# Kernel tuning notes

Measured on AMD Instinct MI355X. Metric: run time of the kernel, lower is better.

## Reference

```python
import jax, jax.numpy as jnp
import numpy as np

N_NODES = 50000
N_EDGES = 800000
D_FEAT = 128
HEADS = 4
C_HID = 64   # n_gat_channels
C_LAST = 64  # fixed in module
ALPHA_LRELU = 0.2


def gat_conv(x, tgt, src, W, a_self, a_neigh, b):
    """Spektral GATConv (single/sparse mode, inference, concat_heads=True)."""
    N = x.shape[0]
    xp = jnp.einsum('nf,fhc->nhc', x, W)                 # [N,H,C] per-head projection
    e_self = jnp.einsum('nhc,hc->nh', xp, a_self)        # [N,H]
    e_neigh = jnp.einsum('nhc,hc->nh', xp, a_neigh)      # [N,H]
    e = jax.nn.leaky_relu(e_self[tgt] + e_neigh[src], ALPHA_LRELU)  # [E,H]
    # segment softmax over incoming edges of each target node
    m = jax.ops.segment_max(e, tgt, num_segments=N)
    m = jnp.where(jnp.isfinite(m), m, 0.0)               # guard empty segments
    ex = jnp.exp(e - m[tgt])
    denom = jax.ops.segment_sum(ex, tgt, num_segments=N)
    alpha = ex / denom[tgt]                               # [E,H]
    msg = alpha[:, :, None] * xp[src]                     # [E,H,C]
    out = jax.ops.segment_sum(msg, tgt, num_segments=N)   # [N,H,C]
    out = out.reshape(N, -1) + b                          # concat heads -> [N,H*C]
    return jax.nn.selu(out)


def setup_inputs() -> dict:
    key = jax.random.key(0)
    ks = jax.random.split(key, 16)
    lecun = lambda k, shape, fan_in: jax.random.normal(k, shape, jnp.float32) * np.sqrt(1.0 / fan_in)
    x = jax.random.normal(ks[0], (N_NODES, D_FEAT), jnp.float32)
    edge_index = jax.random.randint(ks[1], (2, N_EDGES), 0, N_NODES, jnp.int64)
    F1 = HEADS * C_HID
    F2 = HEADS * C_LAST
    return {
        'x': x,
        'edge_index': edge_index,
        'W1': lecun(ks[2], (D_FEAT, HEADS, C_HID), D_FEAT),
        'a_self1': lecun(ks[3], (HEADS, C_HID), C_HID),
        'a_neigh1': lecun(ks[4], (HEADS, C_HID), C_HID),
        'b1': jnp.zeros((F1,), jnp.float32),
        'W2': lecun(ks[5], (F1, HEADS, C_LAST), F1),
        'a_self2': lecun(ks[6], (HEADS, C_LAST), C_LAST),
        'a_neigh2': lecun(ks[7], (HEADS, C_LAST), C_LAST),
        'b2': jnp.zeros((F2,), jnp.float32),
        'Wd1': lecun(ks[8], (F2, 64), F2),
        'bd1': jnp.zeros((64,), jnp.float32),
        'Wd2': lecun(ks[9], (64, 32), 64),
        'bd2': jnp.zeros((32,), jnp.float32),
        'Wo': lecun(ks[10], (32, 1), 32),
        'bo': jnp.zeros((1,), jnp.float32),
    }


def reference(x, edge_index, W1, a_self1, a_neigh1, b1, W2, a_self2, a_neigh2, b2,
              Wd1, bd1, Wd2, bd2, Wo, bo):
    tgt, src = edge_index[0], edge_index[1]
    h = gat_conv(x, tgt, src, W1, a_self1, a_neigh1, b1)   # hidden GATConv (dropout=identity)
    h = gat_conv(h, tgt, src, W2, a_self2, a_neigh2, b2)   # last GATConv
    g = h.sum(axis=0)                                      # GlobalSumPool -> [F2]
    g = jax.nn.selu(g @ Wd1 + bd1)
    g = jax.nn.selu(g @ Wd2 + bd2)
    return g @ Wo + bo                                     # [1]
```

## Files before the change

### kernel.cpp

```cpp
#include <hip/hip_runtime.h>
#include <hip/hip_bf16.h>
#include <hip/hip_fp8.h>
#include <math.h>

#define N_NODES 50000
#define N_EDGES 800000
#define SLOT_CAP 96
#define AGG_BLOCKS (N_NODES / 4)

typedef __attribute__((ext_vector_type(8))) short short8;
typedef __attribute__((ext_vector_type(4))) float f32x4;
typedef __attribute__((ext_vector_type(2))) float f32x2;

__device__ __forceinline__ float selu_f(float x) {
    const float scale = 1.0507009873554805f;
    const float alpha = 1.6732632423543772f;
    return x > 0.f ? scale * x : scale * alpha * (expf(x) - 1.f);
}
__device__ __forceinline__ float lrelu_f(float x) {
    return x >= 0.f ? x : 0.2f * x;
}
__device__ __forceinline__ ushort f2bf(float f) {
    __hip_bfloat16 h = __float2bfloat16(f);
    return *(ushort*)&h;
}
__device__ __forceinline__ unsigned char f2fp8(float f) {
    __hip_fp8_e4m3 q(f);
    return (unsigned char)q.__x;
}
__device__ __forceinline__ float fp82f(unsigned char b) {
    __hip_fp8_e4m3 q; q.__x = (__hip_fp8_storage_t)b;
    return (float)q;
}
__device__ __forceinline__ void fp8x4_decode(unsigned u, float* o) {
#if __has_builtin(__builtin_amdgcn_cvt_pk_f32_fp8)
    f32x2 lo = __builtin_amdgcn_cvt_pk_f32_fp8((int)u, false);
    f32x2 hi = __builtin_amdgcn_cvt_pk_f32_fp8((int)u, true);
    o[0] = lo.x; o[1] = lo.y; o[2] = hi.x; o[3] = hi.y;
#else
    o[0] = fp82f(u & 0xff);
    o[1] = fp82f((u >> 8) & 0xff);
    o[2] = fp82f((u >> 16) & 0xff);
    o[3] = fp82f(u >> 24);
#endif
}
__device__ __forceinline__ unsigned fp8x4_encode(float f0, float f1, float f2, float f3) {
#if __has_builtin(__builtin_amdgcn_cvt_pk_fp8_f32)
    int v = 0;
    v = __builtin_amdgcn_cvt_pk_fp8_f32(f0, f1, v, false);
    v = __builtin_amdgcn_cvt_pk_fp8_f32(f2, f3, v, true);
    return (unsigned)v;
#else
    return (unsigned)f2fp8(f0) | ((unsigned)f2fp8(f1) << 8) |
           ((unsigned)f2fp8(f2) << 16) | ((unsigned)f2fp8(f3) << 24);
#endif
}

__global__ void pack_all(const float* __restrict__ x, ushort* __restrict__ Apx,
                         const float* __restrict__ W1, ushort* __restrict__ Bp1,
                         const float* __restrict__ W2, ushort* __restrict__ Bp2,
                         int* __restrict__ cursor, float* __restrict__ g) {
    int i = blockIdx.x * blockDim.x + threadIdx.x;
    if (i < N_NODES * 128 / 8) {
        const float4* p = (const float4*)x + (size_t)i * 2;
        float4 a = p[0], b = p[1];
        ushort u[8] = { f2bf(a.x), f2bf(a.y), f2bf(a.z), f2bf(a.w),
                        f2bf(b.x), f2bf(b.y), f2bf(b.z), f2bf(b.w) };
        *(uint4*)(Apx + (size_t)i * 8) = *(uint4*)u;
    }
    if (i < 16 * 256) {
        int kg = i >> 8, n = i & 255;
        ushort u[8];
#pragma unroll
        for (int j = 0; j < 8; j++) u[j] = f2bf(W1[(size_t)(kg * 8 + j) * 256 + n]);
        *(uint4*)(Bp1 + ((size_t)kg * 256 + n) * 8) = *(uint4*)u;
    }
    if (i < 32 * 256) {
        int kg = i >> 8, n = i & 255;
        ushort u[8];
#pragma unroll
        for (int j = 0; j < 8; j++) u[j] = f2bf(W2[(size_t)(kg * 8 + j) * 256 + n]);
        *(uint4*)(Bp2 + ((size_t)kg * 256 + n) * 8) = *(uint4*)u;
    }
    if (i < N_NODES) cursor[i] = 0;
    if (i < 256) g[i] = 0.f;
}

__global__ void edge_scatter(const int* __restrict__ tgt, const int* __restrict__ src,
                             int* __restrict__ cursor, int* __restrict__ ssrc, int E) {
    int e = blockIdx.x * blockDim.x + threadIdx.x;
    if (e >= E) return;
    int t = tgt[e];
    int r = atomicAdd(&cursor[t], 1);
    if (r < SLOT_CAP) ssrc[(size_t)t * SLOT_CAP + r] = src[e];
}

__global__ __launch_bounds__(256) void gemm_scores(const short8* __restrict__ A,
                                                   const short8* __restrict__ B,
                                                   unsigned char* __restrict__ C,
                                                   const float* __restrict__ a_self,
                                                   const float* __restrict__ a_neigh,
                                                   float* __restrict__ es,
                                                   float* __restrict__ en,
                                                   int K8, int M) {
    __shared__ short8 Atile[64][5];
    const int tid = threadIdx.x;
    const int wv = tid >> 6, lane = tid & 63;
    const int q = lane >> 4, t = lane & 15;
    const int m0 = blockIdx.x * 64;
    const int n0 = wv * 64;

    const int srow = tid >> 2, sc = tid & 3;
    int grow = m0 + srow; if (grow > M - 1) grow = M - 1;
    const short8* Ag = A + (size_t)grow * K8 + sc;

    f32x4 acc[4][4];
#pragma unroll
    for (int mr = 0; mr < 4; mr++)
#pragma unroll
        for (int nc = 0; nc < 4; nc++) acc[mr][nc] = (f32x4){0.f, 0.f, 0.f, 0.f};

    const short8* Bb = B + (size_t)q * 256 + n0 + t;
    for (int kk = 0; kk < K8; kk += 4) {
        __syncthreads();
        Atile[srow][sc] = Ag[kk];
        __syncthreads();
        short8 a0 = Atile[t][q];
        short8 a1 = Atile[16 + t][q];
        short8 a2 = Atile[32 + t][q];
        short8 a3 = Atile[48 + t][q];
        short8 b0 = Bb[(size_t)kk * 256 + 0];
        short8 b1 = Bb[(size_t)kk * 256 + 16];
        short8 b2 = Bb[(size_t)kk * 256 + 32];
        short8 b3 = Bb[(size_t)kk * 256 + 48];
        acc[0][0] = __builtin_amdgcn_mfma_f32_16x16x32_bf16(a0, b0, acc[0][0], 0, 0, 0);
        acc[0][1] = __builtin_amdgcn_mfma_f32_16x16x32_bf16(a0, b1, acc[0][1], 0, 0, 0);
        acc[0][2] = __builtin_amdgcn_mfma_f32_16x16x32_bf16(a0, b2, acc[0][2], 0, 0, 0);
        acc[0][3] = __builtin_amdgcn_mfma_f32_16x16x32_bf16(a0, b3, acc[0][3], 0, 0, 0);
        acc[1][0] = __builtin_amdgcn_mfma_f32_16x16x32_bf16(a1, b0, acc[1][0], 0, 0, 0);
        acc[1][1] = __builtin_amdgcn_mfma_f32_16x16x32_bf16(a1, b1, acc[1][1], 0, 0, 0);
        acc[1][2] = __builtin_amdgcn_mfma_f32_16x16x32_bf16(a1, b2, acc[1][2], 0, 0, 0);
        acc[1][3] = __builtin_amdgcn_mfma_f32_16x16x32_bf16(a1, b3, acc[1][3], 0, 0, 0);
        acc[2][0] = __builtin_amdgcn_mfma_f32_16x16x32_bf16(a2, b0, acc[2][0], 0, 0, 0);
        acc[2][1] = __builtin_amdgcn_mfma_f32_16x16x32_bf16(a2, b1, acc[2][1], 0, 0, 0);
        acc[2][2] = __builtin_amdgcn_mfma_f32_16x16x32_bf16(a2, b2, acc[2][2], 0, 0, 0);
        acc[2][3] = __builtin_amdgcn_mfma_f32_16x16x32_bf16(a2, b3, acc[2][3], 0, 0, 0);
        acc[3][0] = __builtin_amdgcn_mfma_f32_16x16x32_bf16(a3, b0, acc[3][0], 0, 0, 0);
        acc[3][1] = __builtin_amdgcn_mfma_f32_16x16x32_bf16(a3, b1, acc[3][1], 0, 0, 0);
        acc[3][2] = __builtin_amdgcn_mfma_f32_16x16x32_bf16(a3, b2, acc[3][2], 0, 0, 0);
        acc[3][3] = __builtin_amdgcn_mfma_f32_16x16x32_bf16(a3, b3, acc[3][3], 0, 0, 0);
    }

    unsigned char* Cr = C + n0 + t;
#pragma unroll
    for (int mr = 0; mr < 4; mr++) {
#pragma unroll
        for (int r = 0; r < 4; r++) {
            int row = m0 + mr * 16 + q * 4 + r;
            if (row < M) {
                size_t ro = (size_t)row * 256;
                unsigned pk = fp8x4_encode(acc[mr][0][r], acc[mr][1][r],
                                           acc[mr][2][r], acc[mr][3][r]);
                Cr[ro +  0] = (unsigned char)(pk & 0xff);
                Cr[ro + 16] = (unsigned char)((pk >> 8) & 0xff);
                Cr[ro + 32] = (unsigned char)((pk >> 16) & 0xff);
                Cr[ro + 48] = (unsigned char)(pk >> 24);
            }
        }
    }

    float as[4], an[4];
#pragma unroll
    for (int nc = 0; nc < 4; nc++) {
        as[nc] = a_self[n0 + nc * 16 + t];
        an[nc] = a_neigh[n0 + nc * 16 + t];
    }
#pragma unroll
    for (int mr = 0; mr < 4; mr++) {
#pragma unroll
        for (int r = 0; r < 4; r++) {
            float pes = acc[mr][0][r] * as[0] + acc[mr][1][r] * as[1]
                      + acc[mr][2][r] * as[2] + acc[mr][3][r] * as[3];
            float pen = acc[mr][0][r] * an[0] + acc[mr][1][r] * an[1]
                      + acc[mr][2][r] * an[2] + acc[mr][3][r] * an[3];
#pragma unroll
            for (int mask = 1; mask < 16; mask <<= 1) {
                pes += __shfl_xor(pes, mask);
                pen += __shfl_xor(pen, mask);
            }
            if (t == 0) {
                int row = m0 + mr * 16 + q * 4 + r;
                if (row < M) {
                    es[(size_t)row * 4 + wv] = pes;
                    en[(size_t)row * 4 + wv] = pen;
                }
            }
        }
    }
}

__global__ __launch_bounds__(256) void aggregate(const unsigned char* __restrict__ xp,
                                                 const float* __restrict__ es,
                                                 const float* __restrict__ en,
                                                 const int* __restrict__ cursor,
                                                 const int* __restrict__ ssrc,
                                                 const float* __restrict__ bias,
                                                 ushort* __restrict__ out,
                                                 float* __restrict__ partials, int N) {
    __shared__ float part[4][256];
    int wave = (blockIdx.x * blockDim.x + threadIdx.x) >> 6;
    int wv = (threadIdx.x >> 6) & 3;
    int lane = threadIdx.x & 63;
    if (wave >= N) return;
    int n = wave;
    int e0 = n * SLOT_CAP;
    int deg = cursor[n]; deg = (deg > SLOT_CAP) ? SLOT_CAP : deg;
    int e1 = e0 + deg;
    int h = lane >> 4;
    int c0 = lane * 4;
    float esh = es[(size_t)n * 4 + h];
    float dd = 0.f;
    float a0 = 0.f, a1 = 0.f, a2 = 0.f, a3 = 0.f;
    float b0 = 0.f, b1 = 0.f, b2 = 0.f, b3 = 0.f;
    int e = e0;
    for (; e + 1 < e1; e += 2) {
        int sA = __builtin_amdgcn_readfirstlane(ssrc[e]);
        int sB = __builtin_amdgcn_readfirstlane(ssrc[e + 1]);
        float evA = __expf(lrelu_f(esh + en[(size_t)sA * 4 + h]));
        float evB = __expf(lrelu_f(esh + en[(size_t)sB * 4 + h]));
        unsigned uA = *(const unsigned*)(xp + (size_t)sA * 256 + c0);
        unsigned uB = *(const unsigned*)(xp + (size_t)sB * 256 + c0);
        dd += evA + evB;
        float fA[4], fB[4];
        fp8x4_decode(uA, fA);
        fp8x4_decode(uB, fB);
        a0 += evA * fA[0]; a1 += evA * fA[1]; a2 += evA * fA[2]; a3 += evA * fA[3];
        b0 += evB * fB[0]; b1 += evB * fB[1]; b2 += evB * fB[2]; b3 += evB * fB[3];
    }
    if (e < e1) {
        int s = __builtin_amdgcn_readfirstlane(ssrc[e]);
        float ev = __expf(lrelu_f(esh + en[(size_t)s * 4 + h]));
        unsigned u = *(const unsigned*)(xp + (size_t)s * 256 + c0);
        dd += ev;
        float f[4];
        fp8x4_decode(u, f);
        a0 += ev * f[0]; a1 += ev * f[1]; a2 += ev * f[2]; a3 += ev * f[3];
    }
    float inv = (dd > 0.f) ? 1.f / dd : 0.f;
    float4 bb = *(const float4*)(bias + c0);
    float r0 = selu_f((a0 + b0) * inv + bb.x);
    float r1 = selu_f((a1 + b1) * inv + bb.y);
    float r2 = selu_f((a2 + b2) * inv + bb.z);
    float r3 = selu_f((a3 + b3) * inv + bb.w);
    if (partials == nullptr) {
        ushort r[4] = { f2bf(r0), f2bf(r1), f2bf(r2), f2bf(r3) };
        *(uint2*)(out + (size_t)n * 256 + c0) = *(uint2*)r;
    } else {
        part[wv][c0 + 0] = r0; part[wv][c0 + 1] = r1;
        part[wv][c0 + 2] = r2; part[wv][c0 + 3] = r3;
        __syncthreads();
        if (wv == 0) {
            float4 s;
            s.x = r0 + part[1][c0 + 0] + part[2][c0 + 0] + part[3][c0 + 0];
            s.y = r1 + part[1][c0 + 1] + part[2][c0 + 1] + part[3][c0 + 1];
            s.z = r2 + part[1][c0 + 2] + part[2][c0 + 2] + part[3][c0 + 2];
            s.w = r3 + part[1][c0 + 3] + part[2][c0 + 3] + part[3][c0 + 3];
            *(float4*)(partials + (size_t)blockIdx.x * 256 + c0) = s;
        }
    }
}

__global__ __launch_bounds__(256) void colsum_part(const float* __restrict__ p,
                                                   float* __restrict__ g, int R) {
    __shared__ float part[4][256];
    int tid = threadIdx.x;
    int rg = tid >> 6;
    int c0 = (tid & 63) * 4;
    float4 acc = {0.f, 0.f, 0.f, 0.f};
    for (int r = blockIdx.x * 4 + rg; r < R; r += gridDim.x * 4) {
        float4 v = *(const float4*)(p + (size_t)r * 256 + c0);
        acc.x += v.x; acc.y += v.y; acc.z += v.z; acc.w += v.w;
    }
    *(float4*)(&part[rg][c0]) = acc;
    __syncthreads();
    if (rg == 0) {
        float4 s = acc;
        for (int r = 1; r < 4; r++) {
            s.x += part[r][c0 + 0]; s.y += part[r][c0 + 1];
            s.z += part[r][c0 + 2]; s.w += part[r][c0 + 3];
        }
        atomicAdd(&g[c0 + 0], s.x);
        atomicAdd(&g[c0 + 1], s.y);
        atomicAdd(&g[c0 + 2], s.z);
        atomicAdd(&g[c0 + 3], s.w);
    }
}

__global__ __launch_bounds__(256) void mlp_head(const float* __restrict__ g,
                                                const float* __restrict__ Wd1, const float* __restrict__ bd1,
                                                const float* __restrict__ Wd2, const float* __restrict__ bd2,
                                                const float* __restrict__ Wo, const float* __restrict__ bo,
                                                float* __restrict__ out) {
    __shared__ float sg[256], y1[64], y2[32];
    int t = threadIdx.x;
    sg[t] = g[t];
    __syncthreads();
    if (t < 64) {
        float s = bd1[t];
        for (int k = 0; k < 256; k++) s += sg[k] * Wd1[k * 64 + t];
        y1[t] = selu_f(s);
    }
    __syncthreads();
    if (t < 32) {
        float s = bd2[t];
        for (int k = 0; k < 64; k++) s += y1[k] * Wd2[k * 32 + t];
        y2[t] = selu_f(s);
    }
    __syncthreads();
    if (t == 0) {
        float s = bo[0];
        for (int k = 0; k < 32; k++) s += y2[k] * Wo[k];
        out[0] = s;
    }
}

extern "C" void kernel_launch(void* const* d_in, const int* in_sizes, int n_in,
                              void* d_out, int out_size, void* d_ws, size_t ws_size,
                              hipStream_t stream) {
    const float* x   = (const float*)d_in[0];
    const int*   ei  = (const int*)d_in[1];
    const float* W1  = (const float*)d_in[2];
    const float* as1 = (const float*)d_in[3];
    const float* an1 = (const float*)d_in[4];
    const float* b1  = (const float*)d_in[5];
    const float* W2  = (const float*)d_in[6];
    const float* as2 = (const float*)d_in[7];
    const float* an2 = (const float*)d_in[8];
    const float* b2  = (const float*)d_in[9];
    const float* Wd1 = (const float*)d_in[10];
    const float* bd1 = (const float*)d_in[11];
    const float* Wd2 = (const float*)d_in[12];
    const float* bd2 = (const float*)d_in[13];
    const float* Wo  = (const float*)d_in[14];
    const float* bo  = (const float*)d_in[15];
    const int* tgt  = ei;
    const int* srcp = ei + N_EDGES;

    char* w = (char*)d_ws;
    size_t off_b = 0;
    auto alloc = [&](size_t bytes) -> void* {
        void* p = w + off_b;
        off_b = (off_b + bytes + 255) & ~(size_t)255;
        return p;
    };
    ushort* Apx  = (ushort*)alloc((size_t)N_NODES * 128 * 2);
    ushort* Bp1  = (ushort*)alloc((size_t)128 * 256 * 2);
    ushort* Bp2  = (ushort*)alloc((size_t)256 * 256 * 2);
    unsigned char* xp8 = (unsigned char*)alloc((size_t)N_NODES * 256);
    ushort* h1b  = (ushort*)alloc((size_t)N_NODES * 256 * 2);
    float* es    = (float*)alloc((size_t)N_NODES * 4 * 4);
    float* en    = (float*)alloc((size_t)N_NODES * 4 * 4);
    int*   cursor= (int*)alloc((size_t)N_NODES * 4);
    int*   ssrc  = (int*)alloc((size_t)N_NODES * SLOT_CAP * 4);
    float* pp    = (float*)alloc((size_t)AGG_BLOCKS * 256 * 4);
    float* g     = (float*)alloc(1024);

    const int EB = (N_EDGES + 255) / 256;
    const int GB = (N_NODES + 63) / 64;

    pack_all<<<(N_NODES * 128 / 8 + 255) / 256, 256, 0, stream>>>(
        x, Apx, W1, Bp1, W2, Bp2, cursor, g);

    edge_scatter<<<EB, 256, 0, stream>>>(tgt, srcp, cursor, ssrc, N_EDGES);

    gemm_scores<<<GB, 256, 0, stream>>>((const short8*)Apx, (const short8*)Bp1,
                                        xp8, as1, an1, es, en, 16, N_NODES);
    aggregate<<<AGG_BLOCKS, 256, 0, stream>>>(xp8, es, en, cursor, ssrc, b1, h1b, nullptr, N_NODES);

    gemm_scores<<<GB, 256, 0, stream>>>((const short8*)h1b, (const short8*)Bp2,
                                        xp8, as2, an2, es, en, 32, N_NODES);
    aggregate<<<AGG_BLOCKS, 256, 0, stream>>>(xp8, es, en, cursor, ssrc, b2, nullptr, pp, N_NODES);

    colsum_part<<<128, 256, 0, stream>>>(pp, g, AGG_BLOCKS);
    mlp_head<<<1, 256, 0, stream>>>(g, Wd1, bd1, Wd2, bd2, Wo, bo, (float*)d_out);
}
```

Baseline: 338.1 us.

## Fuse edge scatter with first GEMM launch and batch neighbor index loads in aggregate

Edge scatter and the first projection GEMM now run as one launch, with block ranges split by index, since they are independent. This removes one kernel boundary and lets the two overlap. In aggregate, each lane loads one neighbor index up front and the loop broadcasts it with shuffles, unrolled by four to keep more gathers in flight. Nodes with more than 64 neighbors fall back to the old per-edge loop, and the extra early-exit blocks in the fused launch raise the block count.

```diff
diff --git a/kernel.cpp b/kernel.cpp
--- a/kernel.cpp
+++ b/kernel.cpp
@@ -86,28 +86,20 @@
     if (i < 256) g[i] = 0.f;
 }
 
-__global__ void edge_scatter(const int* __restrict__ tgt, const int* __restrict__ src,
-                             int* __restrict__ cursor, int* __restrict__ ssrc, int E) {
-    int e = blockIdx.x * blockDim.x + threadIdx.x;
-    if (e >= E) return;
-    int t = tgt[e];
-    int r = atomicAdd(&cursor[t], 1);
-    if (r < SLOT_CAP) ssrc[(size_t)t * SLOT_CAP + r] = src[e];
-}
-
-__global__ __launch_bounds__(256) void gemm_scores(const short8* __restrict__ A,
-                                                   const short8* __restrict__ B,
-                                                   unsigned char* __restrict__ C,
-                                                   const float* __restrict__ a_self,
-                                                   const float* __restrict__ a_neigh,
-                                                   float* __restrict__ es,
-                                                   float* __restrict__ en,
-                                                   int K8, int M) {
+__device__ __forceinline__ void gemm_body(int blk,
+                                          const short8* __restrict__ A,
+                                          const short8* __restrict__ B,
+                                          unsigned char* __restrict__ C,
+                                          const float* __restrict__ a_self,
+                                          const float* __restrict__ a_neigh,
+                                          float* __restrict__ es,
+                                          float* __restrict__ en,
+                                          int K8, int M) {
     __shared__ short8 Atile[64][5];
     const int tid = threadIdx.x;
     const int wv = tid >> 6, lane = tid & 63;
     const int q = lane >> 4, t = lane & 15;
-    const int m0 = blockIdx.x * 64;
+    const int m0 = blk * 64;
     const int n0 = wv * 64;
 
     const int srow = tid >> 2, sc = tid & 3;
@@ -199,6 +191,41 @@
     }
 }
 
+__global__ __launch_bounds__(256) void scatter_gemm1(const int* __restrict__ tgt,
+                                                     const int* __restrict__ src,
+                                                     int* __restrict__ cursor,
+                                                     int* __restrict__ ssrc, int E, int EB,
+                                                     const short8* __restrict__ A,
+                                                     const short8* __restrict__ B,
+                                                     unsigned char* __restrict__ C,
+                                                     const float* __restrict__ a_self,
+                                                     const float* __restrict__ a_neigh,
+                                                     float* __restrict__ es,
+                                                     float* __restrict__ en,
+                                                     int K8, int M) {
+    if ((int)blockIdx.x < EB) {
+        int e = blockIdx.x * 256 + threadIdx.x;
+        if (e < E) {
+            int t = tgt[e];
+            int r = atomicAdd(&cursor[t], 1);
+            if (r < SLOT_CAP) ssrc[(size_t)t * SLOT_CAP + r] = src[e];
+        }
+        return;
+    }
+    gemm_body(blockIdx.x - EB, A, B, C, a_self, a_neigh, es, en, K8, M);
+}
+
+__global__ __launch_bounds__(256) void gemm_scores(const short8* __restrict__ A,
+                                                   const short8* __restrict__ B,
+                                                   unsigned char* __restrict__ C,
+                                                   const float* __restrict__ a_self,
+                                                   const float* __restrict__ a_neigh,
+                                                   float* __restrict__ es,
+                                                   float* __restrict__ en,
+                                                   int K8, int M) {
+    gemm_body(blockIdx.x, A, B, C, a_self, a_neigh, es, en, K8, M);
+}
+
 __global__ __launch_bounds__(256) void aggregate(const unsigned char* __restrict__ xp,
                                                  const float* __restrict__ es,
                                                  const float* __restrict__ en,
@@ -215,29 +242,53 @@
     int n = wave;
     int e0 = n * SLOT_CAP;
     int deg = cursor[n]; deg = (deg > SLOT_CAP) ? SLOT_CAP : deg;
-    int e1 = e0 + deg;
     int h = lane >> 4;
     int c0 = lane * 4;
     float esh = es[(size_t)n * 4 + h];
     float dd = 0.f;
     float a0 = 0.f, a1 = 0.f, a2 = 0.f, a3 = 0.f;
-    float b0 = 0.f, b1 = 0.f, b2 = 0.f, b3 = 0.f;
-    int e = e0;
-    for (; e + 1 < e1; e += 2) {
-        int sA = __builtin_amdgcn_readfirstlane(ssrc[e]);
-        int sB = __builtin_amdgcn_readfirstlane(ssrc[e + 1]);
-        float evA = __expf(lrelu_f(esh + en[(size_t)sA * 4 + h]));
-        float evB = __expf(lrelu_f(esh + en[(size_t)sB * 4 + h]));
+
+    int dmain = (deg > 64) ? 64 : deg;
+    int sv = (lane < dmain) ? ssrc[e0 + lane] : 0;
+    int i = 0;
+    for (; i + 3 < dmain; i += 4) {
+        int sA = __shfl(sv, i);
+        int sB = __shfl(sv, i + 1);
+        int sC = __shfl(sv, i + 2);
+        int sD = __shfl(sv, i + 3);
+        float eA = en[(size_t)sA * 4 + h];
+        float eB = en[(size_t)sB * 4 + h];
+        float eC = en[(size_t)sC * 4 + h];
+        float eD = en[(size_t)sD * 4 + h];
         unsigned uA = *(const unsigned*)(xp + (size_t)sA * 256 + c0);
         unsigned uB = *(const unsigned*)(xp + (size_t)sB * 256 + c0);
-        dd += evA + evB;
-        float fA[4], fB[4];
+        unsigned uC = *(const unsigned*)(xp + (size_t)sC * 256 + c0);
+        unsigned uD = *(const unsigned*)(xp + (size_t)sD * 256 + c0);
+        float evA = __expf(lrelu_f(esh + eA));
+        float evB = __expf(lrelu_f(esh + eB));
+        float evC = __expf(lrelu_f(esh + eC));
+        float evD = __expf(lrelu_f(esh + eD));
+        dd += (evA + evB) + (evC + evD);
+        float fA[4], fB[4], fC[4], fD[4];
         fp8x4_decode(uA, fA);
         fp8x4_decode(uB, fB);
-        a0 += evA * fA[0]; a1 += evA * fA[1]; a2 += evA * fA[2]; a3 += evA * fA[3];
-        b0 += evB * fB[0]; b1 += evB * fB[1]; b2 += evB * fB[2]; b3 += evB * fB[3];
-    }
-    if (e < e1) {
+        fp8x4_decode(uC, fC);
+        fp8x4_decode(uD, fD);
+        a0 += evA * fA[0] + evB * fB[0] + evC * fC[0] + evD * fD[0];
+        a1 += evA * fA[1] + evB * fB[1] + evC * fC[1] + evD * fD[1];
+        a2 += evA * fA[2] + evB * fB[2] + evC * fC[2] + evD * fD[2];
+        a3 += evA * fA[3] + evB * fB[3] + evC * fC[3] + evD * fD[3];
+    }
+    for (; i < dmain; i++) {
+        int s = __shfl(sv, i);
+        float ev = __expf(lrelu_f(esh + en[(size_t)s * 4 + h]));
+        unsigned u = *(const unsigned*)(xp + (size_t)s * 256 + c0);
+        dd += ev;
+        float f[4];
+        fp8x4_decode(u, f);
+        a0 += ev * f[0]; a1 += ev * f[1]; a2 += ev * f[2]; a3 += ev * f[3];
+    }
+    for (int e = e0 + 64; e < e0 + deg; e++) {
         int s = __builtin_amdgcn_readfirstlane(ssrc[e]);
         float ev = __expf(lrelu_f(esh + en[(size_t)s * 4 + h]));
         unsigned u = *(const unsigned*)(xp + (size_t)s * 256 + c0);
@@ -246,12 +297,13 @@
         fp8x4_decode(u, f);
         a0 += ev * f[0]; a1 += ev * f[1]; a2 += ev * f[2]; a3 += ev * f[3];
     }
+
     float inv = (dd > 0.f) ? 1.f / dd : 0.f;
     float4 bb = *(const float4*)(bias + c0);
-    float r0 = selu_f((a0 + b0) * inv + bb.x);
-    float r1 = selu_f((a1 + b1) * inv + bb.y);
-    float r2 = selu_f((a2 + b2) * inv + bb.z);
-    float r3 = selu_f((a3 + b3) * inv + bb.w);
+    float r0 = selu_f(a0 * inv + bb.x);
+    float r1 = selu_f(a1 * inv + bb.y);
+    float r2 = selu_f(a2 * inv + bb.z);
+    float r3 = selu_f(a3 * inv + bb.w);
     if (partials == nullptr) {
         ushort r[4] = { f2bf(r0), f2bf(r1), f2bf(r2), f2bf(r3) };
         *(uint2*)(out + (size_t)n * 256 + c0) = *(uint2*)r;
@@ -371,10 +423,9 @@
     pack_all<<<(N_NODES * 128 / 8 + 255) / 256, 256, 0, stream>>>(
         x, Apx, W1, Bp1, W2, Bp2, cursor, g);
 
-    edge_scatter<<<EB, 256, 0, stream>>>(tgt, srcp, cursor, ssrc, N_EDGES);
-
-    gemm_scores<<<GB, 256, 0, stream>>>((const short8*)Apx, (const short8*)Bp1,
-                                        xp8, as1, an1, es, en, 16, N_NODES);
+    scatter_gemm1<<<EB + GB, 256, 0, stream>>>(tgt, srcp, cursor, ssrc, N_EDGES, EB,
+                                               (const short8*)Apx, (const short8*)Bp1,
+                                               xp8, as1, an1, es, en, 16, N_NODES);
     aggregate<<<AGG_BLOCKS, 256, 0, stream>>>(xp8, es, en, cursor, ssrc, b1, h1b, nullptr, N_NODES);
 
     gemm_scores<<<GB, 256, 0, stream>>>((const short8*)h1b, (const short8*)Bp2,
```

Result: faster. 296.8 us (-12.2%).
